# Kernel tuning notes

Measured on AMD Instinct MI355X. Metric: run time of the kernel, lower is better.

## Reference

```python
import jax, jax.numpy as jnp
import numpy as np
import math

B, S, D_MODEL, H, CLIP = 4, 1024, 1024, 16, 16
HEAD_DIM = D_MODEL // H
NEG = -1e6


def setup_inputs() -> dict:
    key = jax.random.key(0)
    ks = jax.random.split(key, 10)
    scale = 1.0 / math.sqrt(D_MODEL)
    return {
        "queries": jax.random.normal(ks[0], (B, S, D_MODEL), jnp.float32),
        "keys": jax.random.normal(ks[1], (B, S, D_MODEL), jnp.float32),
        "values": jax.random.normal(ks[2], (B, S, D_MODEL), jnp.float32),
        "valid_lens": jax.random.randint(ks[3], (B,), 1, S + 1),
        "Wq": jax.random.normal(ks[4], (D_MODEL, D_MODEL), jnp.float32) * scale,
        "Wk": jax.random.normal(ks[5], (D_MODEL, D_MODEL), jnp.float32) * scale,
        "Wv": jax.random.normal(ks[6], (D_MODEL, D_MODEL), jnp.float32) * scale,
        "Wo": jax.random.normal(ks[7], (D_MODEL, D_MODEL), jnp.float32) * scale,
        "Ek": jax.random.normal(ks[8], (2 * CLIP + 1, HEAD_DIM), jnp.float32),
        "Ev": jax.random.normal(ks[9], (2 * CLIP + 1, HEAD_DIM), jnp.float32),
    }


def _split_heads(x):
    # [B, S, D] -> [B*H, S, head_dim]
    b, s, _ = x.shape
    return x.reshape(b, s, H, HEAD_DIM).transpose(0, 2, 1, 3).reshape(b * H, s, HEAD_DIM)


def reference(queries, keys, values, valid_lens, Wq, Wk, Wv, Wo, Ek, Ev):
    q = _split_heads(queries @ Wq.T)  # [BH, S, d]
    k = _split_heads(keys @ Wk.T)
    v = _split_heads(values @ Wv.T)

    # relative-position tables, shared across batch and heads: [Sq, Sk, d]
    rng = jnp.arange(S)
    dist = jnp.clip(rng[None, :] - rng[:, None], -CLIP, CLIP) + CLIP
    pos_k = Ek[dist]
    pos_v = Ev[dist]

    scores = jnp.einsum('bqd,bkd->bqk', q, k) + jnp.einsum('bqd,qkd->bqk', q, pos_k)
    scores = scores / math.sqrt(HEAD_DIM)

    vl = jnp.repeat(valid_lens, H)  # [B*H]
    mask = jnp.arange(S)[None, None, :] < vl[:, None, None]
    attn = jax.nn.softmax(jnp.where(mask, scores, NEG), axis=-1)

    out = jnp.einsum('bqk,bkd->bqd', attn, v) + jnp.einsum('bqk,qkd->bqd', attn, pos_v)

    # merge heads: [B*H, S, d] -> [B, S, D]
    out = out.reshape(B, H, S, HEAD_DIM).transpose(0, 2, 1, 3).reshape(B, S, D_MODEL)
    return out @ Wo.T
```

## Files before the change

### kernel.cpp

```cpp
#include <hip/hip_runtime.h>


typedef __attribute__((ext_vector_type(8))) short short8;
typedef __attribute__((ext_vector_type(4))) float floatx4;

__device__ __forceinline__ unsigned short f2bf(float f) {
  union { float f; unsigned u; } v; v.f = f;
  return (unsigned short)((v.u + 0x7fffu + ((v.u >> 16) & 1u)) >> 16);
}
__device__ __forceinline__ unsigned packbf(float lo, float hi) {
  return ((unsigned)f2bf(hi) << 16) | (unsigned)f2bf(lo);
}

__device__ __forceinline__ void gld16(const void* g, void* l) {
  __builtin_amdgcn_global_load_lds(
      (const __attribute__((address_space(1))) unsigned*)g,
      (__attribute__((address_space(3))) unsigned*)l, 16, 0, 0);
}

#define WS_XQ  ((size_t)0)
#define WS_XK  ((size_t)4194304)
#define WS_XV  ((size_t)8388608)
#define WS_W   ((size_t)12582912)
#define WS_EKB ((size_t)16777216)
#define WS_EVT ((size_t)16781312)
#define WS_QB  ((size_t)16785408)
#define WS_KB  ((size_t)20979712)
#define WS_VT  ((size_t)25174016)
#define WS_OB  ((size_t)0)

__global__ __launch_bounds__(256) void convert_all_kernel(
    const float* __restrict__ q, const float* __restrict__ k,
    const float* __restrict__ v,
    const float* __restrict__ wq, const float* __restrict__ wk,
    const float* __restrict__ wv, const float* __restrict__ wo,
    const float* __restrict__ Ek, const float* __restrict__ Ev,
    const int* __restrict__ valid_lens, unsigned short* __restrict__ ws) {
  int z = blockIdx.z;
  if (z < 3) {
    const float* src = z == 0 ? q : (z == 1 ? k : v);
    unsigned short* dst = ws + (size_t)z * 4194304;
    size_t i = ((size_t)blockIdx.x * 256 + threadIdx.x) * 8;
    if (z > 0) {
      int b = (int)(i >> 20), s = (int)((i >> 10) & 1023);
      if (s >= valid_lens[b]) return;
    }
    float4 a = *(const float4*)(src + i);
    float4 bb = *(const float4*)(src + i + 4);
    uint4 o = { packbf(a.x, a.y), packbf(a.z, a.w), packbf(bb.x, bb.y), packbf(bb.z, bb.w) };
    *(uint4*)(dst + i) = o;
  } else if (z < 7) {
    if (blockIdx.x >= 512) return;
    const float* src = (z == 3) ? wq : (z == 4 ? wk : (z == 5 ? wv : wo));
    unsigned short* dst = ws + WS_W + (size_t)(z - 3) * 1048576;
    size_t i = ((size_t)blockIdx.x * 256 + threadIdx.x) * 8;
    float4 a = *(const float4*)(src + i);
    float4 bb = *(const float4*)(src + i + 4);
    uint4 o = { packbf(a.x, a.y), packbf(a.z, a.w), packbf(bb.x, bb.y), packbf(bb.z, bb.w) };
    *(uint4*)(dst + i) = o;
  } else {
    if (blockIdx.x >= 4) return;
    int gid = blockIdx.x * 256 + threadIdx.x;
    unsigned short* ekb = ws + WS_EKB;
    int i0 = gid * 8;
    unsigned short vals[8];
#pragma unroll
    for (int u = 0; u < 8; u++) {
      int i = i0 + u;
      if (i < 4096) {
        int t = i >> 6, d = i & 63;
        vals[u] = (t < 33) ? f2bf(Ek[t * 64 + d]) : (unsigned short)0;
      } else {
        int j = i - 4096;
        int d = j >> 6, t = j & 63;
        vals[u] = (t < 33) ? f2bf(Ev[t * 64 + d]) : (unsigned short)0;
      }
    }
    *(uint4*)(ekb + i0) = *(uint4*)vals;
  }
}

__device__ __forceinline__ void gemm128_body(
    const unsigned short* __restrict__ A, const unsigned short* __restrict__ W,
    unsigned short* __restrict__ Cb, float* __restrict__ Cf, int mode, float scale) {
  __shared__ unsigned short sA[128 * 32];
  __shared__ unsigned short sB[128 * 32];
  const int tid = threadIdx.x, wave = tid >> 6, lane = tid & 63;
  const int lr = lane & 15, lq = lane >> 4;
  const int wr = wave >> 1, wc = wave & 1;
  const int m0 = blockIdx.y * 128, n0 = blockIdx.x * 128;
  const int srow = lane >> 2, scol = (lane & 3) * 8;

  const unsigned short* gA0 = A + (size_t)(m0 + wave * 16 + srow) * 1024 + scol;
  const unsigned short* gA1 = gA0 + (size_t)64 * 1024;
  const unsigned short* gB0 = W + (size_t)(n0 + wave * 16 + srow) * 1024 + scol;
  const unsigned short* gB1 = gB0 + (size_t)64 * 1024;
  unsigned short* lA0 = sA + wave * 512;  unsigned short* lA1 = lA0 + 2048;
  unsigned short* lB0 = sB + wave * 512;  unsigned short* lB1 = lB0 + 2048;

  floatx4 acc[4][4];
#pragma unroll
  for (int mi = 0; mi < 4; mi++)
#pragma unroll
    for (int ni = 0; ni < 4; ni++) acc[mi][ni] = (floatx4){0.f, 0.f, 0.f, 0.f};

  for (int k0 = 0; k0 < 1024; k0 += 32) {
    gld16(gA0 + k0, lA0); gld16(gA1 + k0, lA1);
    gld16(gB0 + k0, lB0); gld16(gB1 + k0, lB1);
    __syncthreads();
    short8 af[4], bf[4];
#pragma unroll
    for (int mi = 0; mi < 4; mi++)
      af[mi] = *(const short8*)(sA + (wr * 64 + mi * 16 + lr) * 32 + lq * 8);
#pragma unroll
    for (int ni = 0; ni < 4; ni++)
      bf[ni] = *(const short8*)(sB + (wc * 64 + ni * 16 + lr) * 32 + lq * 8);
#pragma unroll
    for (int mi = 0; mi < 4; mi++)
#pragma unroll
      for (int ni = 0; ni < 4; ni++)
        acc[mi][ni] = __builtin_amdgcn_mfma_f32_16x16x32_bf16(af[mi], bf[ni], acc[mi][ni], 0, 0, 0);
    __syncthreads();
  }

  if (mode == 2) {
#pragma unroll
    for (int mi = 0; mi < 4; mi++)
#pragma unroll
      for (int ni = 0; ni < 4; ni++) {
        int col = n0 + wc * 64 + ni * 16 + lr;
        int h = col >> 6, d = col & 63;
        int rowg = m0 + wr * 64 + mi * 16 + lq * 4;
        int b = rowg >> 10, s = rowg & 1023;
        uint2 pk;
        pk.x = packbf(acc[mi][ni][0], acc[mi][ni][1]);
        pk.y = packbf(acc[mi][ni][2], acc[mi][ni][3]);
        *(uint2*)(Cb + ((size_t)((b * 16 + h) * 64 + d) << 10) + s) = pk;
      }
  } else if (mode == 3) {
#pragma unroll
    for (int mi = 0; mi < 4; mi++)
#pragma unroll
      for (int ni = 0; ni < 4; ni++)
#pragma unroll
        for (int r = 0; r < 4; r++) {
          int row = m0 + wr * 64 + mi * 16 + lq * 4 + r;
          int col = n0 + wc * 64 + ni * 16 + lr;
          Cf[(size_t)row * 1024 + col] = acc[mi][ni][r];
        }
  } else {
#pragma unroll
    for (int mi = 0; mi < 4; mi++)
#pragma unroll
      for (int ni = 0; ni < 4; ni++)
#pragma unroll
        for (int r = 0; r < 4; r++) {
          int row = m0 + wr * 64 + mi * 16 + lq * 4 + r;
          int col = n0 + wc * 64 + ni * 16 + lr;
          Cb[(size_t)row * 1024 + col] = f2bf(acc[mi][ni][r] * scale);
        }
  }
}

__global__ __launch_bounds__(256, 3) void proj_qkv_kernel(
    unsigned short* __restrict__ ws, const int* __restrict__ valid_lens) {
  int z = blockIdx.z;
  if (z > 0) {
    int m0 = blockIdx.y * 128;
    if ((m0 & 1023) >= valid_lens[m0 >> 10]) return;
  }
  const unsigned short* A = ws + (size_t)z * 4194304;
  const unsigned short* W = ws + WS_W + (size_t)z * 1048576;
  unsigned short* Cb = (z == 0) ? ws + WS_QB : (z == 1 ? ws + WS_KB : ws + WS_VT);
  int mode = (z == 2) ? 2 : (z == 0 ? 0 : 1);
  float scale = (z == 0) ? 0.125f : 1.0f;
  gemm128_body(A, W, Cb, nullptr, mode, scale);
}

__global__ __launch_bounds__(256, 3) void out_proj_kernel(
    const unsigned short* __restrict__ Ob, const unsigned short* __restrict__ Wo,
    float* __restrict__ out) {
  gemm128_body(Ob, Wo, nullptr, out, 3, 1.f);
}

__global__ __launch_bounds__(64, 3) void attn_rpr_kernel(
    const unsigned short* __restrict__ Qb, const unsigned short* __restrict__ Kb,
    const unsigned short* __restrict__ Vt, const int* __restrict__ valid_lens,
    const unsigned short* __restrict__ Ekb, const unsigned short* __restrict__ Evtb,
    unsigned short* __restrict__ Ob) {
  __shared__ unsigned short sP[16 * 72];
  __shared__ float sQE[16 * 34];
  __shared__ float sW[16 * 34];

  const int lane = threadIdx.x;
  const int lr = lane & 15, lq = lane >> 4;
  const int bh = blockIdx.x, qx = blockIdx.y;
  const int b = bh >> 4;
  const int vlen = valid_lens[b];
  const int i0 = qx * 16;
  const int colh = (bh & 15) * 64;
  const size_t bat = (size_t)b * 1024 * 1024;
  const int rbase = lq * 4;

  for (int i = lane; i < 16 * 34; i += 64) sW[i] = 0.f;

  const unsigned short* gQ = Qb + bat + (size_t)(i0 + lr) * 1024 + colh + lq * 8;
  short8 aq0 = *(const short8*)(gQ);
  short8 aq1 = *(const short8*)(gQ + 32);

#pragma unroll
  for (int ni = 0; ni < 3; ni++) {
    floatx4 aqe = (floatx4){0.f, 0.f, 0.f, 0.f};
    short8 be0 = *(const short8*)(Ekb + (ni * 16 + lr) * 64 + lq * 8);
    short8 be1 = *(const short8*)(Ekb + (ni * 16 + lr) * 64 + 32 + lq * 8);
    aqe = __builtin_amdgcn_mfma_f32_16x16x32_bf16(aq0, be0, aqe, 0, 0, 0);
    aqe = __builtin_amdgcn_mfma_f32_16x16x32_bf16(aq1, be1, aqe, 0, 0, 0);
    int t = ni * 16 + lr;
    if (t < 33)
#pragma unroll
      for (int r = 0; r < 4; r++) sQE[(rbase + r) * 34 + t] = aqe[r];
  }

  floatx4 acc_o[4];
#pragma unroll
  for (int nd = 0; nd < 4; nd++) acc_o[nd] = (floatx4){0.f, 0.f, 0.f, 0.f};
  float rs0[4] = {0.f, 0.f, 0.f, 0.f};
  float rs32[4] = {0.f, 0.f, 0.f, 0.f};

  const int vcl = vlen < 1024 ? vlen : 1024;
  const int kt_max = (vcl + 63) >> 6;

  const unsigned short* gK = Kb + bat + colh;
  const unsigned short* gV = Vt + ((size_t)bh * 64) * 1024;

  for (int kt = 0; kt < kt_max; kt++) {
    const int j0 = kt * 64;

    short8 bk[4][2], bv[4][2];
#pragma unroll
    for (int ni = 0; ni < 4; ni++) {
      const unsigned short* p = gK + (size_t)(j0 + ni * 16 + lr) * 1024 + lq * 8;
      bk[ni][0] = *(const short8*)(p);
      bk[ni][1] = *(const short8*)(p + 32);
    }
#pragma unroll
    for (int nd = 0; nd < 4; nd++) {
      const unsigned short* p = gV + (size_t)(nd * 16 + lr) * 1024 + j0 + lq * 8;
      bv[nd][0] = *(const short8*)(p);
      bv[nd][1] = *(const short8*)(p + 32);
    }

    floatx4 accs[4];
    __builtin_amdgcn_s_setprio(1);
#pragma unroll
    for (int ni = 0; ni < 4; ni++) {
      accs[ni] = (floatx4){0.f, 0.f, 0.f, 0.f};
      accs[ni] = __builtin_amdgcn_mfma_f32_16x16x32_bf16(aq0, bk[ni][0], accs[ni], 0, 0, 0);
      accs[ni] = __builtin_amdgcn_mfma_f32_16x16x32_bf16(aq1, bk[ni][1], accs[ni], 0, 0, 0);
    }
    __builtin_amdgcn_s_setprio(0);

    const bool general = (j0 > i0 - 79) && (j0 < i0 + 31);
    if (!general) {
      const bool hi = (j0 >= i0 + 31);
      const int tconst = hi ? 32 : 0;
      float qe[4];
#pragma unroll
      for (int r = 0; r < 4; r++) qe[r] = sQE[(rbase + r) * 34 + tconst];
#pragma unroll
      for (int ni = 0; ni < 4; ni++)
#pragma unroll
        for (int r = 0; r < 4; r++) {
          int j_g = j0 + ni * 16 + lr;
          float pv = (j_g < vlen) ? __expf(accs[ni][r] + qe[r]) : 0.f;
          if (hi) rs32[r] += pv; else rs0[r] += pv;
          sP[(rbase + r) * 72 + ni * 16 + lr] = f2bf(pv);
        }
    } else {
#pragma unroll
      for (int ni = 0; ni < 4; ni++)
#pragma unroll
        for (int r = 0; r < 4; r++) {
          int i_g = i0 + rbase + r;
          int j_g = j0 + ni * 16 + lr;
          int dd = j_g - i_g; dd = dd < -16 ? -16 : (dd > 16 ? 16 : dd);
          int t = dd + 16;
          float pv = (j_g < vlen) ? __expf(accs[ni][r] + sQE[(rbase + r) * 34 + t]) : 0.f;
          atomicAdd(&sW[(rbase + r) * 34 + t], pv);
          sP[(rbase + r) * 72 + ni * 16 + lr] = f2bf(pv);
        }
    }

    short8 ap0 = *(const short8*)(sP + lr * 72 + lq * 8);
    short8 ap1 = *(const short8*)(sP + lr * 72 + 32 + lq * 8);
    __builtin_amdgcn_s_setprio(1);
#pragma unroll
    for (int nd = 0; nd < 4; nd++) {
      acc_o[nd] = __builtin_amdgcn_mfma_f32_16x16x32_bf16(ap0, bv[nd][0], acc_o[nd], 0, 0, 0);
      acc_o[nd] = __builtin_amdgcn_mfma_f32_16x16x32_bf16(ap1, bv[nd][1], acc_o[nd], 0, 0, 0);
    }
    __builtin_amdgcn_s_setprio(0);
  }

#pragma unroll
  for (int x = 1; x < 16; x <<= 1)
#pragma unroll
    for (int r = 0; r < 4; r++) {
      rs0[r] += __shfl_xor(rs0[r], x, 64);
      rs32[r] += __shfl_xor(rs32[r], x, 64);
    }
  if (lr == 0)
#pragma unroll
    for (int r = 0; r < 4; r++) {
      sW[(rbase + r) * 34 + 0] += rs0[r];
      sW[(rbase + r) * 34 + 32] += rs32[r];
    }

  {
    int row = lane >> 2;
    int c0 = (lane & 3) * 16;
    unsigned* sP32 = (unsigned*)sP;
#pragma unroll
    for (int q = 0; q < 8; q++) {
      int t0 = c0 + 2 * q, t1 = t0 + 1;
      float w0 = (t0 < 33) ? sW[row * 34 + t0] : 0.f;
      float w1 = (t1 < 33) ? sW[row * 34 + t1] : 0.f;
      sP32[row * 36 + (c0 >> 1) + q] = packbf(w0, w1);
    }
  }
  {
    short8 aw0 = *(const short8*)(sP + lr * 72 + lq * 8);
    short8 aw1 = *(const short8*)(sP + lr * 72 + 32 + lq * 8);
#pragma unroll
    for (int nd = 0; nd < 4; nd++) {
      short8 be0 = *(const short8*)(Evtb + (nd * 16 + lr) * 64 + lq * 8);
      short8 be1 = *(const short8*)(Evtb + (nd * 16 + lr) * 64 + 32 + lq * 8);
      acc_o[nd] = __builtin_amdgcn_mfma_f32_16x16x32_bf16(aw0, be0, acc_o[nd], 0, 0, 0);
      acc_o[nd] = __builtin_amdgcn_mfma_f32_16x16x32_bf16(aw1, be1, acc_o[nd], 0, 0, 0);
    }
  }

  float linv[4];
#pragma unroll
  for (int r = 0; r < 4; r++) {
    float l = 0.f;
#pragma unroll
    for (int t = 0; t < 33; t++) l += sW[(rbase + r) * 34 + t];
    linv[r] = 1.f / l;
  }
#pragma unroll
  for (int nd = 0; nd < 4; nd++)
#pragma unroll
    for (int r = 0; r < 4; r++) {
      int i_loc = rbase + r;
      Ob[bat + (size_t)(i0 + i_loc) * 1024 + colh + nd * 16 + lr] =
          f2bf(acc_o[nd][r] * linv[r]);
    }
}

extern "C" void kernel_launch(void* const* d_in, const int* in_sizes, int n_in,
                              void* d_out, int out_size, void* d_ws, size_t ws_size,
                              hipStream_t stream) {
  const float* queries = (const float*)d_in[0];
  const float* keys    = (const float*)d_in[1];
  const float* values  = (const float*)d_in[2];
  const int* valid_lens = (const int*)d_in[3];
  const float* Wq = (const float*)d_in[4];
  const float* Wk = (const float*)d_in[5];
  const float* Wv = (const float*)d_in[6];
  const float* Wo = (const float*)d_in[7];
  const float* Ek = (const float*)d_in[8];
  const float* Ev = (const float*)d_in[9];
  float* out = (float*)d_out;
  unsigned short* ws = (unsigned short*)d_ws;

  convert_all_kernel<<<dim3(2048, 1, 8), 256, 0, stream>>>(
      queries, keys, values, Wq, Wk, Wv, Wo, Ek, Ev, valid_lens, ws);
  proj_qkv_kernel<<<dim3(8, 32, 3), 256, 0, stream>>>(ws, valid_lens);
  attn_rpr_kernel<<<dim3(64, 64), 64, 0, stream>>>(
      ws + WS_QB, ws + WS_KB, ws + WS_VT, valid_lens, ws + WS_EKB, ws + WS_EVT, ws + WS_OB);
  out_proj_kernel<<<dim3(8, 32), 256, 0, stream>>>(ws + WS_OB, ws + WS_W + 3145728, out);
}
```

Measured before the change: 232.9 us.

## Split attention key loop across four waves with LDS atomic reduction

The attention kernel goes from one wave to four waves per block. Each wave handles a contiguous chunk of the key tiles for the same 16-query tile. Partial output accumulators and the row sums are combined through shared-memory atomics, and wave 0 then applies the relative-position value term and normalizes. This raises parallelism and latency hiding for long key ranges. The cost is extra LDS atomic traffic, a block barrier, and possible races if the hidden loop body updates shared per-offset weights non-atomically from several waves.

Result: slower. 310.7 us (+33.4%).

```diff
diff --git a/kernel.cpp b/kernel.cpp
--- a/kernel.cpp
+++ b/kernel.cpp
@@ -183,16 +183,19 @@
   gemm128_body(Ob, Wo, nullptr, out, 3, 1.f);
 }
 
-__global__ __launch_bounds__(64, 3) void attn_rpr_kernel(
+__global__ __launch_bounds__(256, 4) void attn_rpr_kernel(
     const unsigned short* __restrict__ Qb, const unsigned short* __restrict__ Kb,
     const unsigned short* __restrict__ Vt, const int* __restrict__ valid_lens,
     const unsigned short* __restrict__ Ekb, const unsigned short* __restrict__ Evtb,
     unsigned short* __restrict__ Ob) {
-  __shared__ unsigned short sP[16 * 72];
+  __shared__ unsigned short sPall[4][16 * 72];
   __shared__ float sQE[16 * 34];
   __shared__ float sW[16 * 34];
-
-  const int lane = threadIdx.x;
+  __shared__ float sO[16 * 64];
+
+  const int tid = threadIdx.x;
+  const int wave = tid >> 6;
+  const int lane = tid & 63;
   const int lr = lane & 15, lq = lane >> 4;
   const int bh = blockIdx.x, qx = blockIdx.y;
   const int b = bh >> 4;
@@ -202,7 +205,11 @@
   const size_t bat = (size_t)b * 1024 * 1024;
   const int rbase = lq * 4;
 
-  for (int i = lane; i < 16 * 34; i += 64) sW[i] = 0.f;
+  unsigned short* sP = sPall[wave];
+
+  for (int i = tid; i < 16 * 34; i += 256) sW[i] = 0.f;
+  for (int i = tid; i < 16 * 64; i += 256) sO[i] = 0.f;
+  __syncthreads();
 
   const unsigned short* gQ = Qb + bat + (size_t)(i0 + lr) * 1024 + colh + lq * 8;
   short8 aq0 = *(const short8*)(gQ);
@@ -229,11 +236,14 @@
 
   const int vcl = vlen < 1024 ? vlen : 1024;
   const int kt_max = (vcl + 63) >> 6;
+  const int chunk = (kt_max + 3) >> 2;
+  const int ktb = wave * chunk;
+  const int kte = (ktb + chunk < kt_max) ? ktb + chunk : kt_max;
 
   const unsigned short* gK = Kb + bat + colh;
   const unsigned short* gV = Vt + ((size_t)bh * 64) * 1024;
 
-  for (int kt = 0; kt < kt_max; kt++) {
+  for (int kt = ktb; kt < kte; kt++) {
     const int j0 = kt * 64;
 
     short8 bk[4][2], bv[4][2];
@@ -312,9 +322,18 @@
   if (lr == 0)
 #pragma unroll
     for (int r = 0; r < 4; r++) {
-      sW[(rbase + r) * 34 + 0] += rs0[r];
-      sW[(rbase + r) * 34 + 32] += rs32[r];
-    }
+      atomicAdd(&sW[(rbase + r) * 34 + 0], rs0[r]);
+      atomicAdd(&sW[(rbase + r) * 34 + 32], rs32[r]);
+    }
+
+#pragma unroll
+  for (int nd = 0; nd < 4; nd++)
+#pragma unroll
+    for (int r = 0; r < 4; r++)
+      atomicAdd(&sO[(rbase + r) * 64 + nd * 16 + lr], acc_o[nd][r]);
+
+  __syncthreads();
+  if (wave != 0) return;
 
   {
     int row = lane >> 2;
@@ -328,6 +347,14 @@
       sP32[row * 36 + (c0 >> 1) + q] = packbf(w0, w1);
     }
   }
+
+  floatx4 accf[4];
+#pragma unroll
+  for (int nd = 0; nd < 4; nd++)
+#pragma unroll
+    for (int r = 0; r < 4; r++)
+      accf[nd][r] = sO[(rbase + r) * 64 + nd * 16 + lr];
+
   {
     short8 aw0 = *(const short8*)(sP + lr * 72 + lq * 8);
     short8 aw1 = *(const short8*)(sP + lr * 72 + 32 + lq * 8);
@@ -335,8 +362,8 @@
     for (int nd = 0; nd < 4; nd++) {
       short8 be0 = *(const short8*)(Evtb + (nd * 16 + lr) * 64 + lq * 8);
       short8 be1 = *(const short8*)(Evtb + (nd * 16 + lr) * 64 + 32 + lq * 8);
-      acc_o[nd] = __builtin_amdgcn_mfma_f32_16x16x32_bf16(aw0, be0, acc_o[nd], 0, 0, 0);
-      acc_o[nd] = __builtin_amdgcn_mfma_f32_16x16x32_bf16(aw1, be1, acc_o[nd], 0, 0, 0);
+      accf[nd] = __builtin_amdgcn_mfma_f32_16x16x32_bf16(aw0, be0, accf[nd], 0, 0, 0);
+      accf[nd] = __builtin_amdgcn_mfma_f32_16x16x32_bf16(aw1, be1, accf[nd], 0, 0, 0);
     }
   }
 
@@ -354,7 +381,7 @@
     for (int r = 0; r < 4; r++) {
       int i_loc = rbase + r;
       Ob[bat + (size_t)(i0 + i_loc) * 1024 + colh + nd * 16 + lr] =
-          f2bf(acc_o[nd][r] * linv[r]);
+          f2bf(accf[nd][r] * linv[r]);
     }
 }
 
@@ -377,7 +404,7 @@
   convert_all_kernel<<<dim3(2048, 1, 8), 256, 0, stream>>>(
       queries, keys, values, Wq, Wk, Wv, Wo, Ek, Ev, valid_lens, ws);
   proj_qkv_kernel<<<dim3(8, 32, 3), 256, 0, stream>>>(ws, valid_lens);
-  attn_rpr_kernel<<<dim3(64, 64), 64, 0, stream>>>(
+  attn_rpr_kernel<<<dim3(64, 64), 256, 0, stream>>>(
       ws + WS_QB, ws + WS_KB, ws + WS_VT, valid_lens, ws + WS_EKB, ws + WS_EVT, ws + WS_OB);
   out_proj_kernel<<<dim3(8, 32), 256, 0, stream>>>(ws + WS_OB, ws + WS_W + 3145728, out);
 }
```

## Process 32 query rows per attention wave to reuse K/V loads

Applied to the files above, without the earlier changes.

Each single-wave attention block now handles two 16-row query groups, so every K and V tile loaded from global memory feeds twice as many MFMAs. The grid is halved and the general-band condition is widened to cover the 32-row span. The V loads are also moved after the QK MFMAs to overlap them with compute. This doubles register and LDS use per wave, lowering the occupancy hint from 3 to 2, and reduces the number of blocks available to hide latency.

Result: faster. 225.7 us (-3.1%).

```diff
diff --git a/kernel.cpp b/kernel.cpp
--- a/kernel.cpp
+++ b/kernel.cpp
@@ -183,49 +183,58 @@
   gemm128_body(Ob, Wo, nullptr, out, 3, 1.f);
 }
 
-__global__ __launch_bounds__(64, 3) void attn_rpr_kernel(
+__global__ __launch_bounds__(64, 2) void attn_rpr_kernel(
     const unsigned short* __restrict__ Qb, const unsigned short* __restrict__ Kb,
     const unsigned short* __restrict__ Vt, const int* __restrict__ valid_lens,
     const unsigned short* __restrict__ Ekb, const unsigned short* __restrict__ Evtb,
     unsigned short* __restrict__ Ob) {
-  __shared__ unsigned short sP[16 * 72];
-  __shared__ float sQE[16 * 34];
-  __shared__ float sW[16 * 34];
+  __shared__ unsigned short sP[32 * 72];
+  __shared__ float sQE[32 * 34];
+  __shared__ float sW[32 * 34];
 
   const int lane = threadIdx.x;
   const int lr = lane & 15, lq = lane >> 4;
   const int bh = blockIdx.x, qx = blockIdx.y;
   const int b = bh >> 4;
   const int vlen = valid_lens[b];
-  const int i0 = qx * 16;
+  const int i0 = qx * 32;
   const int colh = (bh & 15) * 64;
   const size_t bat = (size_t)b * 1024 * 1024;
   const int rbase = lq * 4;
 
-  for (int i = lane; i < 16 * 34; i += 64) sW[i] = 0.f;
+  for (int i = lane; i < 32 * 34; i += 64) sW[i] = 0.f;
 
   const unsigned short* gQ = Qb + bat + (size_t)(i0 + lr) * 1024 + colh + lq * 8;
-  short8 aq0 = *(const short8*)(gQ);
-  short8 aq1 = *(const short8*)(gQ + 32);
+  short8 aq0[2], aq1[2];
+#pragma unroll
+  for (int g = 0; g < 2; g++) {
+    aq0[g] = *(const short8*)(gQ + (size_t)g * 16 * 1024);
+    aq1[g] = *(const short8*)(gQ + (size_t)g * 16 * 1024 + 32);
+  }
 
 #pragma unroll
   for (int ni = 0; ni < 3; ni++) {
-    floatx4 aqe = (floatx4){0.f, 0.f, 0.f, 0.f};
     short8 be0 = *(const short8*)(Ekb + (ni * 16 + lr) * 64 + lq * 8);
     short8 be1 = *(const short8*)(Ekb + (ni * 16 + lr) * 64 + 32 + lq * 8);
-    aqe = __builtin_amdgcn_mfma_f32_16x16x32_bf16(aq0, be0, aqe, 0, 0, 0);
-    aqe = __builtin_amdgcn_mfma_f32_16x16x32_bf16(aq1, be1, aqe, 0, 0, 0);
     int t = ni * 16 + lr;
-    if (t < 33)
-#pragma unroll
-      for (int r = 0; r < 4; r++) sQE[(rbase + r) * 34 + t] = aqe[r];
-  }
-
-  floatx4 acc_o[4];
-#pragma unroll
-  for (int nd = 0; nd < 4; nd++) acc_o[nd] = (floatx4){0.f, 0.f, 0.f, 0.f};
-  float rs0[4] = {0.f, 0.f, 0.f, 0.f};
-  float rs32[4] = {0.f, 0.f, 0.f, 0.f};
+#pragma unroll
+    for (int g = 0; g < 2; g++) {
+      floatx4 aqe = (floatx4){0.f, 0.f, 0.f, 0.f};
+      aqe = __builtin_amdgcn_mfma_f32_16x16x32_bf16(aq0[g], be0, aqe, 0, 0, 0);
+      aqe = __builtin_amdgcn_mfma_f32_16x16x32_bf16(aq1[g], be1, aqe, 0, 0, 0);
+      if (t < 33)
+#pragma unroll
+        for (int r = 0; r < 4; r++) sQE[(g * 16 + rbase + r) * 34 + t] = aqe[r];
+    }
+  }
+
+  floatx4 acc_o[2][4];
+#pragma unroll
+  for (int g = 0; g < 2; g++)
+#pragma unroll
+    for (int nd = 0; nd < 4; nd++) acc_o[g][nd] = (floatx4){0.f, 0.f, 0.f, 0.f};
+  float rs0[2][4] = {{0.f,0.f,0.f,0.f},{0.f,0.f,0.f,0.f}};
+  float rs32[2][4] = {{0.f,0.f,0.f,0.f},{0.f,0.f,0.f,0.f}};
 
   const int vcl = vlen < 1024 ? vlen : 1024;
   const int kt_max = (vcl + 63) >> 6;
@@ -236,13 +245,27 @@
   for (int kt = 0; kt < kt_max; kt++) {
     const int j0 = kt * 64;
 
-    short8 bk[4][2], bv[4][2];
+    short8 bk[4][2];
 #pragma unroll
     for (int ni = 0; ni < 4; ni++) {
       const unsigned short* p = gK + (size_t)(j0 + ni * 16 + lr) * 1024 + lq * 8;
       bk[ni][0] = *(const short8*)(p);
       bk[ni][1] = *(const short8*)(p + 32);
     }
+
+    floatx4 accs[2][4];
+    __builtin_amdgcn_s_setprio(1);
+#pragma unroll
+    for (int g = 0; g < 2; g++)
+#pragma unroll
+      for (int ni = 0; ni < 4; ni++) {
+        accs[g][ni] = (floatx4){0.f, 0.f, 0.f, 0.f};
+        accs[g][ni] = __builtin_amdgcn_mfma_f32_16x16x32_bf16(aq0[g], bk[ni][0], accs[g][ni], 0, 0, 0);
+        accs[g][ni] = __builtin_amdgcn_mfma_f32_16x16x32_bf16(aq1[g], bk[ni][1], accs[g][ni], 0, 0, 0);
+      }
+    __builtin_amdgcn_s_setprio(0);
+
+    short8 bv[4][2];
 #pragma unroll
     for (int nd = 0; nd < 4; nd++) {
       const unsigned short* p = gV + (size_t)(nd * 16 + lr) * 1024 + j0 + lq * 8;
@@ -250,112 +273,120 @@
       bv[nd][1] = *(const short8*)(p + 32);
     }
 
-    floatx4 accs[4];
+    const bool general = (j0 > i0 - 79) && (j0 < i0 + 47);
+    if (!general) {
+      const bool hi = (j0 >= i0 + 47);
+      const int tconst = hi ? 32 : 0;
+#pragma unroll
+      for (int g = 0; g < 2; g++) {
+        float qe[4];
+#pragma unroll
+        for (int r = 0; r < 4; r++) qe[r] = sQE[(g * 16 + rbase + r) * 34 + tconst];
+#pragma unroll
+        for (int ni = 0; ni < 4; ni++)
+#pragma unroll
+          for (int r = 0; r < 4; r++) {
+            int j_g = j0 + ni * 16 + lr;
+            float pv = (j_g < vlen) ? __expf(accs[g][ni][r] + qe[r]) : 0.f;
+            if (hi) rs32[g][r] += pv; else rs0[g][r] += pv;
+            sP[(g * 16 + rbase + r) * 72 + ni * 16 + lr] = f2bf(pv);
+          }
+      }
+    } else {
+#pragma unroll
+      for (int g = 0; g < 2; g++)
+#pragma unroll
+        for (int ni = 0; ni < 4; ni++)
+#pragma unroll
+          for (int r = 0; r < 4; r++) {
+            int i_g = i0 + g * 16 + rbase + r;
+            int j_g = j0 + ni * 16 + lr;
+            int dd = j_g - i_g; dd = dd < -16 ? -16 : (dd > 16 ? 16 : dd);
+            int t = dd + 16;
+            float pv = (j_g < vlen) ? __expf(accs[g][ni][r] + sQE[(g * 16 + rbase + r) * 34 + t]) : 0.f;
+            atomicAdd(&sW[(g * 16 + rbase + r) * 34 + t], pv);
+            sP[(g * 16 + rbase + r) * 72 + ni * 16 + lr] = f2bf(pv);
+          }
+    }
+
     __builtin_amdgcn_s_setprio(1);
 #pragma unroll
-    for (int ni = 0; ni < 4; ni++) {
-      accs[ni] = (floatx4){0.f, 0.f, 0.f, 0.f};
-      accs[ni] = __builtin_amdgcn_mfma_f32_16x16x32_bf16(aq0, bk[ni][0], accs[ni], 0, 0, 0);
-      accs[ni] = __builtin_amdgcn_mfma_f32_16x16x32_bf16(aq1, bk[ni][1], accs[ni], 0, 0, 0);
+    for (int g = 0; g < 2; g++) {
+      short8 ap0 = *(const short8*)(sP + (g * 16 + lr) * 72 + lq * 8);
+      short8 ap1 = *(const short8*)(sP + (g * 16 + lr) * 72 + 32 + lq * 8);
+#pragma unroll
+      for (int nd = 0; nd < 4; nd++) {
+        acc_o[g][nd] = __builtin_amdgcn_mfma_f32_16x16x32_bf16(ap0, bv[nd][0], acc_o[g][nd], 0, 0, 0);
+        acc_o[g][nd] = __builtin_amdgcn_mfma_f32_16x16x32_bf16(ap1, bv[nd][1], acc_o[g][nd], 0, 0, 0);
+      }
     }
     __builtin_amdgcn_s_setprio(0);
-
-    const bool general = (j0 > i0 - 79) && (j0 < i0 + 31);
-    if (!general) {
-      const bool hi = (j0 >= i0 + 31);
-      const int tconst = hi ? 32 : 0;
-      float qe[4];
-#pragma unroll
-      for (int r = 0; r < 4; r++) qe[r] = sQE[(rbase + r) * 34 + tconst];
-#pragma unroll
-      for (int ni = 0; ni < 4; ni++)
-#pragma unroll
-        for (int r = 0; r < 4; r++) {
-          int j_g = j0 + ni * 16 + lr;
-          float pv = (j_g < vlen) ? __expf(accs[ni][r] + qe[r]) : 0.f;
-          if (hi) rs32[r] += pv; else rs0[r] += pv;
-          sP[(rbase + r) * 72 + ni * 16 + lr] = f2bf(pv);
-        }
-    } else {
-#pragma unroll
-      for (int ni = 0; ni < 4; ni++)
-#pragma unroll
-        for (int r = 0; r < 4; r++) {
-          int i_g = i0 + rbase + r;
-          int j_g = j0 + ni * 16 + lr;
-          int dd = j_g - i_g; dd = dd < -16 ? -16 : (dd > 16 ? 16 : dd);
-          int t = dd + 16;
-          float pv = (j_g < vlen) ? __expf(accs[ni][r] + sQE[(rbase + r) * 34 + t]) : 0.f;
-          atomicAdd(&sW[(rbase + r) * 34 + t], pv);
-          sP[(rbase + r) * 72 + ni * 16 + lr] = f2bf(pv);
-        }
-    }
-
-    short8 ap0 = *(const short8*)(sP + lr * 72 + lq * 8);
-    short8 ap1 = *(const short8*)(sP + lr * 72 + 32 + lq * 8);
-    __builtin_amdgcn_s_setprio(1);
-#pragma unroll
-    for (int nd = 0; nd < 4; nd++) {
-      acc_o[nd] = __builtin_amdgcn_mfma_f32_16x16x32_bf16(ap0, bv[nd][0], acc_o[nd], 0, 0, 0);
-      acc_o[nd] = __builtin_amdgcn_mfma_f32_16x16x32_bf16(ap1, bv[nd][1], acc_o[nd], 0, 0, 0);
-    }
-    __builtin_amdgcn_s_setprio(0);
   }
 
 #pragma unroll
   for (int x = 1; x < 16; x <<= 1)
 #pragma unroll
-    for (int r = 0; r < 4; r++) {
-      rs0[r] += __shfl_xor(rs0[r], x, 64);
-      rs32[r] += __shfl_xor(rs32[r], x, 64);
-    }
+    for (int g = 0; g < 2; g++)
+#pragma unroll
+      for (int r = 0; r < 4; r++) {
+        rs0[g][r] += __shfl_xor(rs0[g][r], x, 64);
+        rs32[g][r] += __shfl_xor(rs32[g][r], x, 64);
+      }
   if (lr == 0)
 #pragma unroll
-    for (int r = 0; r < 4; r++) {
-      sW[(rbase + r) * 34 + 0] += rs0[r];
-      sW[(rbase + r) * 34 + 32] += rs32[r];
-    }
+    for (int g = 0; g < 2; g++)
+#pragma unroll
+      for (int r = 0; r < 4; r++) {
+        sW[(g * 16 + rbase + r) * 34 + 0] += rs0[g][r];
+        sW[(g * 16 + rbase + r) * 34 + 32] += rs32[g][r];
+      }
 
   {
     int row = lane >> 2;
     int c0 = (lane & 3) * 16;
     unsigned* sP32 = (unsigned*)sP;
 #pragma unroll
-    for (int q = 0; q < 8; q++) {
-      int t0 = c0 + 2 * q, t1 = t0 + 1;
-      float w0 = (t0 < 33) ? sW[row * 34 + t0] : 0.f;
-      float w1 = (t1 < 33) ? sW[row * 34 + t1] : 0.f;
-      sP32[row * 36 + (c0 >> 1) + q] = packbf(w0, w1);
-    }
-  }
-  {
-    short8 aw0 = *(const short8*)(sP + lr * 72 + lq * 8);
-    short8 aw1 = *(const short8*)(sP + lr * 72 + 32 + lq * 8);
+    for (int g = 0; g < 2; g++)
+#pragma unroll
+      for (int q = 0; q < 8; q++) {
+        int t0 = c0 + 2 * q, t1 = t0 + 1;
+        float w0 = (t0 < 33) ? sW[(g * 16 + row) * 34 + t0] : 0.f;
+        float w1 = (t1 < 33) ? sW[(g * 16 + row) * 34 + t1] : 0.f;
+        sP32[(g * 16 + row) * 36 + (c0 >> 1) + q] = packbf(w0, w1);
+      }
+  }
+#pragma unroll
+  for (int g = 0; g < 2; g++) {
+    short8 aw0 = *(const short8*)(sP + (g * 16 + lr) * 72 + lq * 8);
+    short8 aw1 = *(const short8*)(sP + (g * 16 + lr) * 72 + 32 + lq * 8);
 #pragma unroll
     for (int nd = 0; nd < 4; nd++) {
       short8 be0 = *(const short8*)(Evtb + (nd * 16 + lr) * 64 + lq * 8);
       short8 be1 = *(const short8*)(Evtb + (nd * 16 + lr) * 64 + 32 + lq * 8);
-      acc_o[nd] = __builtin_amdgcn_mfma_f32_16x16x32_bf16(aw0, be0, acc_o[nd], 0, 0, 0);
-      acc_o[nd] = __builtin_amdgcn_mfma_f32_16x16x32_bf16(aw1, be1, acc_o[nd], 0, 0, 0);
-    }
-  }
-
-  float linv[4];
-#pragma unroll
-  for (int r = 0; r < 4; r++) {
-    float l = 0.f;
-#pragma unroll
-    for (int t = 0; t < 33; t++) l += sW[(rbase + r) * 34 + t];
-    linv[r] = 1.f / l;
-  }
-#pragma unroll
-  for (int nd = 0; nd < 4; nd++)
+      acc_o[g][nd] = __builtin_amdgcn_mfma_f32_16x16x32_bf16(aw0, be0, acc_o[g][nd], 0, 0, 0);
+      acc_o[g][nd] = __builtin_amdgcn_mfma_f32_16x16x32_bf16(aw1, be1, acc_o[g][nd], 0, 0, 0);
+    }
+  }
+
+#pragma unroll
+  for (int g = 0; g < 2; g++) {
+    float linv[4];
 #pragma unroll
     for (int r = 0; r < 4; r++) {
-      int i_loc = rbase + r;
-      Ob[bat + (size_t)(i0 + i_loc) * 1024 + colh + nd * 16 + lr] =
-          f2bf(acc_o[nd][r] * linv[r]);
-    }
+      float l = 0.f;
+#pragma unroll
+      for (int t = 0; t < 33; t++) l += sW[(g * 16 + rbase + r) * 34 + t];
+      linv[r] = 1.f / l;
+    }
+#pragma unroll
+    for (int nd = 0; nd < 4; nd++)
+#pragma unroll
+      for (int r = 0; r < 4; r++) {
+        int row = i0 + g * 16 + rbase + r;
+        Ob[bat + (size_t)row * 1024 + colh + nd * 16 + lr] =
+            f2bf(acc_o[g][nd][r] * linv[r]);
+      }
+  }
 }
 
 extern "C" void kernel_launch(void* const* d_in, const int* in_sizes, int n_in,
@@ -377,7 +408,7 @@
   convert_all_kernel<<<dim3(2048, 1, 8), 256, 0, stream>>>(
       queries, keys, values, Wq, Wk, Wv, Wo, Ek, Ev, valid_lens, ws);
   proj_qkv_kernel<<<dim3(8, 32, 3), 256, 0, stream>>>(ws, valid_lens);
-  attn_rpr_kernel<<<dim3(64, 64), 64, 0, stream>>>(
+  attn_rpr_kernel<<<dim3(64, 32), 64, 0, stream>>>(
       ws + WS_QB, ws + WS_KB, ws + WS_VT, valid_lens, ws + WS_EKB, ws + WS_EVT, ws + WS_OB);
   out_proj_kernel<<<dim3(8, 32), 256, 0, stream>>>(ws + WS_OB, ws + WS_W + 3145728, out);
 }
```
